# Kernel optimization log

Measured on AMD Instinct MI355X. Metric: run time of the kernel, lower is better.

The kernel has to match this reference:

```python
import jax, jax.numpy as jnp
import numpy as np

N, F, H, E = 20000, 512, 8, 320000
D = F // H
SCALING = D ** (-0.5)


def _layernorm(x, g, b, eps=1e-5):
    mu = jnp.mean(x, axis=-1, keepdims=True)
    var = jnp.var(x, axis=-1, keepdims=True)
    return (x - mu) * jax.lax.rsqrt(var + eps) * g + b


def setup_inputs() -> dict:
    key = jax.random.key(0)
    ks = jax.random.split(key, 12)
    feat = jax.random.normal(ks[0], (N, F), dtype=jnp.float32)
    edge_src = jax.random.randint(ks[1], (E,), 0, N, dtype=jnp.int32)
    edge_dst = jax.random.randint(ks[2], (E,), 0, N, dtype=jnp.int32)
    # self-loops on the first N edges so every node has in-degree >= 1
    loops = jnp.arange(N, dtype=jnp.int32)
    edge_src = edge_src.at[:N].set(loops)
    edge_dst = edge_dst.at[:N].set(loops)
    s = 1.0 / np.sqrt(F)
    def w(k, shape, scale=s):
        return jax.random.normal(k, shape, dtype=jnp.float32) * scale
    return {
        "feat": feat, "edge_src": edge_src, "edge_dst": edge_dst,
        "Wq": w(ks[3], (F, F)), "Wk": w(ks[4], (F, F)), "Wv": w(ks[5], (F, F)),
        "Wnode": w(ks[6], (F, F)), "Wskip": w(ks[7], (F, F)),
        "Wgate": w(ks[8], (3 * F, 1), scale=1.0 / np.sqrt(3 * F)),
        "ln1_g": jnp.ones((F,), jnp.float32), "ln1_b": jnp.zeros((F,), jnp.float32),
        "ln2_g": jnp.ones((F,), jnp.float32), "ln2_b": jnp.zeros((F,), jnp.float32),
        "W1": w(ks[9], (F, F)), "W2": w(ks[10], (F, F)),
    }


def reference(feat, edge_src, edge_dst, Wq, Wk, Wv, Wnode, Wskip, Wgate,
              ln1_g, ln1_b, ln2_g, ln2_b, W1, W2):
    # --- attention (GraphMultiAttentionV2, use_efeats=False, eval mode) ---
    q = (feat @ Wq).reshape(N, H, D)
    k = (feat @ Wk).reshape(N, H, D)
    v = (feat @ Wv).reshape(N, H, D)
    # u_dot_v: per-edge per-head dot product  [E, H]
    logits = jnp.einsum('ehd,ehd->eh', q[edge_src], k[edge_dst])
    logits = jnp.clip(logits, -5.0, 5.0) / SCALING  # faithful: a / scaling
    # edge softmax grouped by destination node
    m = jax.ops.segment_max(logits, edge_dst, num_segments=N)  # [N, H]
    ex = jnp.exp(logits - m[edge_dst])
    denom = jax.ops.segment_sum(ex, edge_dst, num_segments=N)
    sa = ex / denom[edge_dst]  # [E, H]
    # u_mul_e + sum aggregation
    msg = v[edge_src] * sa[..., None]  # [E, H, D]
    agg = jax.ops.segment_sum(msg, edge_dst, num_segments=N).reshape(N, F)
    rst = agg @ Wnode
    # --- gated residual ---
    skip = feat @ Wskip
    gate = jax.nn.sigmoid(jnp.concatenate([rst, skip, rst - skip], axis=-1) @ Wgate)
    h = _layernorm(rst * gate + skip * (1.0 - gate), ln1_g, ln1_b)
    # --- FFN + residual ---
    ffn = jax.nn.relu(_layernorm(h, ln2_g, ln2_b) @ W1) @ W2
    return h + ffn
```

## Files before the change

### kernel.cpp

```cpp
#include <hip/hip_runtime.h>
#include <hip/hip_bf16.h>
#include <hip/hip_fp16.h>

#define NN 20000
#define FD 512
#define NH 8
#define NE 320000
#define MP 20096

typedef unsigned int u32;
typedef unsigned short u16;
typedef __bf16 bf16x8 __attribute__((ext_vector_type(8)));
typedef _Float16 f16x8 __attribute__((ext_vector_type(8)));
typedef float f32x4 __attribute__((ext_vector_type(4)));

#define AS1 __attribute__((address_space(1)))
#define AS3 __attribute__((address_space(3)))

__device__ __forceinline__ u16 f2bf(float f) {
  __hip_bfloat16 h = __float2bfloat16(f);
  union { __hip_bfloat16 b; u16 u; } c; c.b = h; return c.u;
}
__device__ __forceinline__ float bf2f(u32 u) { return __uint_as_float(u << 16); }
__device__ __forceinline__ u16 f2h(float f) {
  union { __half h; u16 u; } c; c.h = __float2half(f); return c.u;
}
__device__ __forceinline__ void gl_lds16(const void* g, void* l) {
  __builtin_amdgcn_global_load_lds((AS1 void*)const_cast<void*>(g), (AS3 void*)l, 16, 0, 0);
}
__device__ __forceinline__ void up_h4(uint2 w, float* f) {
  union { u32 u; __half2 h; } c;
  c.u = w.x; float2 t0 = __half22float2(c.h); f[0]=t0.x; f[1]=t0.y;
  c.u = w.y; float2 t1 = __half22float2(c.h); f[2]=t1.x; f[3]=t1.y;
}

__global__ __launch_bounds__(256) void k_wprep(const float* __restrict__ feat,
    const float* __restrict__ Wq, const float* __restrict__ Wk,
    const float* __restrict__ Wv, const float* __restrict__ Wsk,
    const float* __restrict__ Wn, const float* __restrict__ W1,
    const float* __restrict__ W2, const float* __restrict__ Wg,
    const int* __restrict__ e_dst,
    u16* __restrict__ Af, u16* __restrict__ Bqkvs, u16* __restrict__ Bnt,
    u16* __restrict__ B1t, u16* __restrict__ B2t,
    float* __restrict__ gA, float* __restrict__ gB, int* __restrict__ deg)
{
  int idx = blockIdx.x * 256 + threadIdx.x;
  if (idx < MP * FD / 4) {
    size_t i = (size_t)idx * 4;
    float4 v = make_float4(0.f, 0.f, 0.f, 0.f);
    if (i < (size_t)NN * FD) v = *(const float4*)(feat + i);
    *(ushort4*)(Af + i) = make_ushort4(f2h(v.x), f2h(v.y), f2h(v.z), f2h(v.w));
    return;
  }
  idx -= MP * FD / 4;
  if (idx < 2048 * 512) {
    int n = idx >> 9, k = idx & 511;
    float v;
    if (n < 1024) {
      int j = n & 7, dim = (n >> 3) * 4 + (j & 3);
      v = (j < 4) ? Wq[k * 512 + dim] : Wv[k * 512 + dim];
    } else if (n < 1536) v = Wk[k * 512 + (n - 1024)];
    else                 v = Wsk[k * 512 + (n - 1536)];
    Bqkvs[idx] = f2h(v);
    return;
  }
  idx -= 2048 * 512;
  if (idx < 512 * 512) { int n = idx >> 9, k = idx & 511; Bnt[idx] = f2bf(Wn[k * 512 + n]); return; }
  idx -= 512 * 512;
  if (idx < 512 * 512) { int n = idx >> 9, k = idx & 511; B1t[idx] = f2bf(W1[k * 512 + n]); return; }
  idx -= 512 * 512;
  if (idx < 512 * 512) { int n = idx >> 9, k = idx & 511; B2t[idx] = f2bf(W2[k * 512 + n]); return; }
  idx -= 512 * 512;
  if (idx < 512) {
    gA[idx] = Wg[idx] + Wg[2 * 512 + idx];
    gB[idx] = Wg[512 + idx] - Wg[2 * 512 + idx];
    return;
  }
  idx -= 512;
  if (idx < NE) atomicAdd(&deg[e_dst[idx]], 1);
}

template<int NCOLS, int MODE, int FP16>
__global__ __launch_bounds__(256, 4) void k_gemm(
    const u16* __restrict__ A, const u16* __restrict__ B,
    float* __restrict__ Cf, u16* __restrict__ Cb, u16* __restrict__ Cb2,
    u16* __restrict__ Cb3, int Mreal)
{
  const long brow = (long)blockIdx.x * 128;
  if (brow >= MP) return;
  __shared__ u16 sA[2][128 * 32];
  __shared__ u16 sB[2][128 * 32];
  const int tid = threadIdx.x, lane = tid & 63, w = tid >> 6;
  const int wr = w >> 1, wc = w & 1;
  const long bcol = (long)blockIdx.y * 128;
  const int srl = tid >> 2, scl = (tid & 3) * 8;

  auto stage = [&](int b, int kt) {
#pragma unroll
    for (int s = 0; s < 2; s++) {
      gl_lds16(A + (brow + s * 64 + srl) * FD + kt + scl, &sA[b][s * 2048 + w * 512]);
      gl_lds16(B + (bcol + s * 64 + srl) * FD + kt + scl, &sB[b][s * 2048 + w * 512]);
    }
  };

  f32x4 acc[4][4] = {};
  stage(0, 0);
  __syncthreads();
  int cur = 0;
  const int ro = (lane >> 4) * 8;
  for (int kt = 0; kt < FD; kt += 32) {
    if (kt + 32 < FD) stage(cur ^ 1, kt + 32);
#pragma unroll
    for (int m = 0; m < 4; m++) {
      const u16* pa = &sA[cur][(wr * 64 + m * 16 + (lane & 15)) * 32 + ro];
#pragma unroll
      for (int n = 0; n < 4; n++) {
        const u16* pb = &sB[cur][(wc * 64 + n * 16 + (lane & 15)) * 32 + ro];
        if constexpr (FP16)
          acc[m][n] = __builtin_amdgcn_mfma_f32_16x16x32_f16(
              *(const f16x8*)pa, *(const f16x8*)pb, acc[m][n], 0, 0, 0);
        else
          acc[m][n] = __builtin_amdgcn_mfma_f32_16x16x32_bf16(
              *(const bf16x8*)pa, *(const bf16x8*)pb, acc[m][n], 0, 0, 0);
      }
    }
    __syncthreads();
    cur ^= 1;
  }
#pragma unroll
  for (int m = 0; m < 4; m++) {
    long row0 = brow + wr * 64 + m * 16 + (lane >> 4) * 4;
#pragma unroll
    for (int n = 0; n < 4; n++) {
      long col = bcol + wc * 64 + n * 16 + (lane & 15);
#pragma unroll
      for (int j = 0; j < 4; j++) {
        long row = row0 + j;
        if (row < Mreal) {
          float v = acc[m][n][j];
          if constexpr (MODE == 1) Cb[row * NCOLS + col] = f2bf(fmaxf(v, 0.f));
          else if constexpr (MODE == 2) Cb[row * NCOLS + col] = f2bf(v);
          else if constexpr (MODE == 6) {
            if (col < 1024)      Cb[row * 1024 + col] = f2h(v);
            else if (col < 1536) Cb2[row * 512 + (col - 1024)] = f2h(v);
            else                 Cb3[row * 512 + (col - 1536)] = f2bf(v);
          } else {
            long o = row * NCOLS + col;
            Cf[o] = bf2f((u32)Cb2[o]) + v;
          }
        }
      }
    }
  }
}

__global__ __launch_bounds__(1024) void k_scan(const int* __restrict__ deg, int* __restrict__ offa)
{
  __shared__ int wsum[16];
  const int tid = threadIdx.x, lane = tid & 63, wid = tid >> 6;
  const int base = tid * 20;
  int loc[20];
  int s = 0;
#pragma unroll
  for (int j = 0; j < 20; j++) {
    int i = base + j;
    int v = (i < NN) ? deg[i] : 0;
    s += v; loc[j] = s;
  }
  int incl = s;
#pragma unroll
  for (int d = 1; d < 64; d <<= 1) { int t = __shfl_up(incl, d); if (lane >= d) incl += t; }
  if (lane == 63) wsum[wid] = incl;
  __syncthreads();
  if (tid < 16) {
    int ws = wsum[tid];
#pragma unroll
    for (int d = 1; d < 16; d <<= 1) { int t = __shfl_up(ws, d, 16); if (tid >= d) ws += t; }
    wsum[tid] = ws;
  }
  __syncthreads();
  int prev = incl - s + (wid ? wsum[wid - 1] : 0);
  if (tid == 0) offa[0] = 0;
#pragma unroll
  for (int j = 0; j < 20; j++) {
    int i = base + j;
    if (i < NN) offa[i + 1] = prev + loc[j];
  }
}

__global__ __launch_bounds__(256) void k_scatter(const int* __restrict__ src, const int* __restrict__ dst,
    const int* __restrict__ offa, int* __restrict__ cnt, int* __restrict__ esrcs)
{
  int e = blockIdx.x * 256 + threadIdx.x;
  if (e >= NE) return;
  int d = dst[e];
  int p = offa[d] + atomicAdd(&cnt[d], 1);
  esrcs[p] = src[e];
}

__global__ __launch_bounds__(256) void k_edge(const int* __restrict__ offa,
    const int* __restrict__ esrcs, const u16* __restrict__ QV,
    const u16* __restrict__ Kb, u16* __restrict__ aggb)
{
  int wid = blockIdx.x * 4 + (threadIdx.x >> 6);
  int nd = wid >> 1, half = wid & 1;
  int lane = threadIdx.x & 63;
  if (nd >= MP) return;
  const int g = half * 64 + lane;
  u16* op = aggb + (size_t)nd * FD + g * 4;
  if (nd >= NN) { *(ushort4*)op = make_ushort4(0, 0, 0, 0); return; }
  uint2 kw = *(const uint2*)(Kb + (size_t)nd * 512 + g * 4);
  float kx[4]; up_h4(kw, kx);
  int b0 = offa[nd], b1 = offa[nd + 1];
  float den = 0.f, a0 = 0.f, a1 = 0.f, a2 = 0.f, a3 = 0.f;
  for (int p = b0; p < b1; p += 8) {
    int ss[8]; uint4 qv[8];
#pragma unroll
    for (int u = 0; u < 8; u++) { int ix = p + u; ss[u] = esrcs[ix < b1 ? ix : b1 - 1]; }
#pragma unroll
    for (int u = 0; u < 8; u++)
      qv[u] = *(const uint4*)(QV + (size_t)ss[u] * 1024 + g * 8);
#pragma unroll
    for (int u = 0; u < 8; u++) {
      float qx[4]; up_h4(make_uint2(qv[u].x, qv[u].y), qx);
      float d = qx[0]*kx[0] + qx[1]*kx[1] + qx[2]*kx[2] + qx[3]*kx[3];
      d += __shfl_xor(d, 1); d += __shfl_xor(d, 2);
      d += __shfl_xor(d, 4); d += __shfl_xor(d, 8);
      float ex = __expf(fminf(fmaxf(d, -5.f), 5.f) * 8.f - 40.f);
      ex = (p + u < b1) ? ex : 0.f;
      den += ex;
      float vx[4]; up_h4(make_uint2(qv[u].z, qv[u].w), vx);
      a0 += ex * vx[0]; a1 += ex * vx[1]; a2 += ex * vx[2]; a3 += ex * vx[3];
    }
  }
  float rd = 1.f / den;
  *(ushort4*)op = make_ushort4(f2bf(a0*rd), f2bf(a1*rd), f2bf(a2*rd), f2bf(a3*rd));
}

__device__ __forceinline__ float blkred(float v, float* sb)
{
#pragma unroll
  for (int s = 1; s < 64; s <<= 1) v += __shfl_xor(v, s);
  __syncthreads();
  if ((threadIdx.x & 63) == 0) sb[threadIdx.x >> 6] = v;
  __syncthreads();
  return sb[0] + sb[1];
}

__global__ __launch_bounds__(128) void k_gate_ln(const u16* __restrict__ rstb, const u16* __restrict__ skpb,
    const float* __restrict__ gA, const float* __restrict__ gB,
    const float* __restrict__ g1, const float* __restrict__ b1,
    const float* __restrict__ g2, const float* __restrict__ b2,
    u16* __restrict__ hb, u16* __restrict__ h2b)
{
  __shared__ float sb[2];
  const int t = threadIdx.x;
  const size_t base = (size_t)blockIdx.x * FD + t * 4;
  ushort4 ru = *(const ushort4*)(rstb + base);
  ushort4 su = *(const ushort4*)(skpb + base);
  float r0 = bf2f(ru.x), r1 = bf2f(ru.y), r2 = bf2f(ru.z), r3 = bf2f(ru.w);
  float s0 = bf2f(su.x), s1 = bf2f(su.y), s2 = bf2f(su.z), s3 = bf2f(su.w);
  float4 av = *(const float4*)(gA + t * 4);
  float4 bv = *(const float4*)(gB + t * 4);
  float gd = r0*av.x + r1*av.y + r2*av.z + r3*av.w
           + s0*bv.x + s1*bv.y + s2*bv.z + s3*bv.w;
  float tot = blkred(gd, sb);
  float g = 1.f / (1.f + __expf(-tot));
  float x0 = g*r0 + (1.f-g)*s0;
  float x1 = g*r1 + (1.f-g)*s1;
  float x2 = g*r2 + (1.f-g)*s2;
  float x3 = g*r3 + (1.f-g)*s3;
  float m1 = blkred(x0+x1+x2+x3, sb) * (1.f/FD);
  float d0 = x0-m1, d1 = x1-m1, d2 = x2-m1, d3 = x3-m1;
  float v1 = blkred(d0*d0+d1*d1+d2*d2+d3*d3, sb) * (1.f/FD);
  float rs = rsqrtf(v1 + 1e-5f);
  float4 G1 = *(const float4*)(g1 + t*4);
  float4 Bb1 = *(const float4*)(b1 + t*4);
  float h0 = d0*rs*G1.x + Bb1.x;
  float h1 = d1*rs*G1.y + Bb1.y;
  float h2 = d2*rs*G1.z + Bb1.z;
  float h3 = d3*rs*G1.w + Bb1.w;
  *(ushort4*)(hb + base) = make_ushort4(f2bf(h0), f2bf(h1), f2bf(h2), f2bf(h3));
  float m2 = blkred(h0+h1+h2+h3, sb) * (1.f/FD);
  float e0 = h0-m2, e1 = h1-m2, e2 = h2-m2, e3 = h3-m2;
  float v2 = blkred(e0*e0+e1*e1+e2*e2+e3*e3, sb) * (1.f/FD);
  float rs2 = rsqrtf(v2 + 1e-5f);
  float4 G2 = *(const float4*)(g2 + t*4);
  float4 Bb2 = *(const float4*)(b2 + t*4);
  *(ushort4*)(h2b + base) = make_ushort4(
      f2bf(e0*rs2*G2.x + Bb2.x), f2bf(e1*rs2*G2.y + Bb2.y),
      f2bf(e2*rs2*G2.z + Bb2.z), f2bf(e3*rs2*G2.w + Bb2.w));
}

extern "C" void kernel_launch(void* const* d_in, const int* in_sizes, int n_in,
                              void* d_out, int out_size, void* d_ws, size_t ws_size,
                              hipStream_t stream)
{
  const float* feat = (const float*)d_in[0];
  const int* e_src = (const int*)d_in[1];
  const int* e_dst = (const int*)d_in[2];
  const float* Wq  = (const float*)d_in[3];
  const float* Wk  = (const float*)d_in[4];
  const float* Wv  = (const float*)d_in[5];
  const float* Wn  = (const float*)d_in[6];
  const float* Wsk = (const float*)d_in[7];
  const float* Wg  = (const float*)d_in[8];
  const float* l1g = (const float*)d_in[9];
  const float* l1b = (const float*)d_in[10];
  const float* l2g = (const float*)d_in[11];
  const float* l2b = (const float*)d_in[12];
  const float* W1  = (const float*)d_in[13];
  const float* W2  = (const float*)d_in[14];

  char* ws = (char*)d_ws;
  size_t o = 0;
  auto al = [&](size_t b) { char* r = ws + o; o = (o + b + 255) & ~(size_t)255; return r; };

  u16* Af    = (u16*)al((size_t)MP * FD * 2);
  u16* Bqkvs = (u16*)al((size_t)2048 * FD * 2);
  u16* Bnt   = (u16*)al((size_t)FD * FD * 2);
  u16* B1t   = (u16*)al((size_t)FD * FD * 2);
  u16* B2t   = (u16*)al((size_t)FD * FD * 2);
  float* gA  = (float*)al(FD * 4);
  float* gB  = (float*)al(FD * 4);
  u16* QV    = (u16*)al((size_t)MP * 1024 * 2);
  u16* Kb    = (u16*)al((size_t)MP * FD * 2);
  u16* SKIPb = (u16*)al((size_t)MP * FD * 2);
  u16* aggb  = (u16*)al((size_t)MP * FD * 2);
  u16* h2b   = (u16*)al((size_t)MP * FD * 2);
  u16* hb    = (u16*)al((size_t)MP * FD * 2);
  int* deg   = (int*)al((size_t)2 * NN * 4);
  int* cnt   = deg + NN;
  int* offa  = (int*)al((size_t)(NN + 1) * 4);
  int* esrcs = (int*)al((size_t)NE * 4);
  if (o > ws_size) return;
  u16* rstb = Kb;
  u16* midb = Af;
  float* out = (float*)d_out;

  hipMemsetAsync(deg, 0, (size_t)2 * NN * 4, stream);

  {
    int total = MP * FD / 4 + 2048 * 512 + 3 * 512 * 512 + 512 + NE;
    k_wprep<<<dim3((total + 255) / 256), 256, 0, stream>>>(feat, Wq, Wk, Wv, Wsk, Wn, W1, W2, Wg,
        e_dst, Af, Bqkvs, Bnt, B1t, B2t, gA, gB, deg);
  }

  k_gemm<2048, 6, 1><<<dim3(160, 16), 256, 0, stream>>>(Af, Bqkvs, nullptr, QV, Kb, SKIPb, MP);

  k_scan<<<dim3(1), 1024, 0, stream>>>(deg, offa);
  k_scatter<<<dim3((NE + 255) / 256), 256, 0, stream>>>(e_src, e_dst, offa, cnt, esrcs);
  k_edge<<<dim3(MP / 2), 256, 0, stream>>>(offa, esrcs, QV, Kb, aggb);

  k_gemm<512, 2, 0><<<dim3(160, 4), 256, 0, stream>>>(aggb, Bnt, nullptr, rstb, nullptr, nullptr, MP);
  k_gate_ln<<<dim3(NN), 128, 0, stream>>>(rstb, SKIPb, gA, gB, l1g, l1b, l2g, l2b, hb, h2b);
  k_gemm<512, 1, 0><<<dim3(160, 4), 256, 0, stream>>>(h2b, B1t, nullptr, midb, nullptr, nullptr, NN);
  k_gemm<512, 7, 0><<<dim3(160, 4), 256, 0, stream>>>(midb, B2t, out, nullptr, hb, nullptr, NN);
}
```

Measured before the change: 315.7 us.

## Fold second layernorm into W1 GEMM epilogue and use wave-per-row gate LN

The second layernorm is folded algebraically into the FFN's first GEMM. W1 is pre-scaled by ln2 gamma, per-row rstd and rstd*mean are computed in the gate kernel, and the GEMM epilogue applies rs*acc - rs*mean*(g·W1) + (b·W1). This removes the h2b write and read. The gate/LN kernel is also restructured so one wavefront handles a row with shuffle-only reductions and single-pass mean/variance, replacing 128-thread blocks with repeated block barriers. The trade-offs are more bf16 rounding error, since h is rounded before the GEMM while the statistics come from fp32, and a serial 512-length dot-product loop added to the prep kernel.

```diff
diff --git a/kernel.cpp b/kernel.cpp
--- a/kernel.cpp
+++ b/kernel.cpp
@@ -33,16 +33,24 @@
   c.u = w.x; float2 t0 = __half22float2(c.h); f[0]=t0.x; f[1]=t0.y;
   c.u = w.y; float2 t1 = __half22float2(c.h); f[2]=t1.x; f[3]=t1.y;
 }
+__device__ __forceinline__ void up_b8(uint4 w, float* f) {
+  f[0]=bf2f(w.x & 0xffffu); f[1]=bf2f(w.x >> 16);
+  f[2]=bf2f(w.y & 0xffffu); f[3]=bf2f(w.y >> 16);
+  f[4]=bf2f(w.z & 0xffffu); f[5]=bf2f(w.z >> 16);
+  f[6]=bf2f(w.w & 0xffffu); f[7]=bf2f(w.w >> 16);
+}
 
 __global__ __launch_bounds__(256) void k_wprep(const float* __restrict__ feat,
     const float* __restrict__ Wq, const float* __restrict__ Wk,
     const float* __restrict__ Wv, const float* __restrict__ Wsk,
     const float* __restrict__ Wn, const float* __restrict__ W1,
     const float* __restrict__ W2, const float* __restrict__ Wg,
+    const float* __restrict__ l2g, const float* __restrict__ l2b,
     const int* __restrict__ e_dst,
     u16* __restrict__ Af, u16* __restrict__ Bqkvs, u16* __restrict__ Bnt,
     u16* __restrict__ B1t, u16* __restrict__ B2t,
-    float* __restrict__ gA, float* __restrict__ gB, int* __restrict__ deg)
+    float* __restrict__ gA, float* __restrict__ gB,
+    float* __restrict__ uw, int* __restrict__ deg)
 {
   int idx = blockIdx.x * 256 + threadIdx.x;
   if (idx < MP * FD / 4) {
@@ -67,7 +75,8 @@
   idx -= 2048 * 512;
   if (idx < 512 * 512) { int n = idx >> 9, k = idx & 511; Bnt[idx] = f2bf(Wn[k * 512 + n]); return; }
   idx -= 512 * 512;
-  if (idx < 512 * 512) { int n = idx >> 9, k = idx & 511; B1t[idx] = f2bf(W1[k * 512 + n]); return; }
+  if (idx < 512 * 512) { int n = idx >> 9, k = idx & 511;
+    B1t[idx] = f2bf(l2g[k] * W1[k * 512 + n]); return; }
   idx -= 512 * 512;
   if (idx < 512 * 512) { int n = idx >> 9, k = idx & 511; B2t[idx] = f2bf(W2[k * 512 + n]); return; }
   idx -= 512 * 512;
@@ -77,6 +86,15 @@
     return;
   }
   idx -= 512;
+  if (idx < 1024) {
+    int j = idx & 511;
+    const float* vec = (idx < 512) ? l2g : l2b;
+    float acc = 0.f;
+    for (int c = 0; c < 512; c++) acc += vec[c] * W1[c * 512 + j];
+    uw[idx] = acc;
+    return;
+  }
+  idx -= 1024;
   if (idx < NE) atomicAdd(&deg[e_dst[idx]], 1);
 }
 
@@ -127,6 +145,7 @@
     __syncthreads();
     cur ^= 1;
   }
+  const float* uwp = (const float*)Cb2;
 #pragma unroll
   for (int m = 0; m < 4; m++) {
     long row0 = brow + wr * 64 + m * 16 + (lane >> 4) * 4;
@@ -138,15 +157,17 @@
         long row = row0 + j;
         if (row < Mreal) {
           float v = acc[m][n][j];
-          if constexpr (MODE == 1) Cb[row * NCOLS + col] = f2bf(fmaxf(v, 0.f));
-          else if constexpr (MODE == 2) Cb[row * NCOLS + col] = f2bf(v);
+          if constexpr (MODE == 2) Cb[row * NCOLS + col] = f2bf(v);
           else if constexpr (MODE == 6) {
             if (col < 1024)      Cb[row * 1024 + col] = f2h(v);
             else if (col < 1536) Cb2[row * 512 + (col - 1024)] = f2h(v);
             else                 Cb3[row * 512 + (col - 1536)] = f2bf(v);
-          } else {
+          } else if constexpr (MODE == 7) {
             long o = row * NCOLS + col;
             Cf[o] = bf2f((u32)Cb2[o]) + v;
+          } else {
+            float val = Cf[row] * v - Cf[NN + row] * uwp[col] + uwp[512 + col];
+            Cb[row * NCOLS + col] = f2bf(fmaxf(val, 0.f));
           }
         }
       }
@@ -237,59 +258,67 @@
   *(ushort4*)op = make_ushort4(f2bf(a0*rd), f2bf(a1*rd), f2bf(a2*rd), f2bf(a3*rd));
 }
 
-__device__ __forceinline__ float blkred(float v, float* sb)
-{
-#pragma unroll
-  for (int s = 1; s < 64; s <<= 1) v += __shfl_xor(v, s);
-  __syncthreads();
-  if ((threadIdx.x & 63) == 0) sb[threadIdx.x >> 6] = v;
-  __syncthreads();
-  return sb[0] + sb[1];
-}
-
-__global__ __launch_bounds__(128) void k_gate_ln(const u16* __restrict__ rstb, const u16* __restrict__ skpb,
-    const float* __restrict__ gA, const float* __restrict__ gB,
+__global__ __launch_bounds__(256) void k_gate_ln(const u16* __restrict__ rstb,
+    const u16* __restrict__ skpb, const float* __restrict__ gA, const float* __restrict__ gB,
     const float* __restrict__ g1, const float* __restrict__ b1,
-    const float* __restrict__ g2, const float* __restrict__ b2,
-    u16* __restrict__ hb, u16* __restrict__ h2b)
-{
-  __shared__ float sb[2];
-  const int t = threadIdx.x;
-  const size_t base = (size_t)blockIdx.x * FD + t * 4;
-  ushort4 ru = *(const ushort4*)(rstb + base);
-  ushort4 su = *(const ushort4*)(skpb + base);
-  float r0 = bf2f(ru.x), r1 = bf2f(ru.y), r2 = bf2f(ru.z), r3 = bf2f(ru.w);
-  float s0 = bf2f(su.x), s1 = bf2f(su.y), s2 = bf2f(su.z), s3 = bf2f(su.w);
-  float4 av = *(const float4*)(gA + t * 4);
-  float4 bv = *(const float4*)(gB + t * 4);
-  float gd = r0*av.x + r1*av.y + r2*av.z + r3*av.w
-           + s0*bv.x + s1*bv.y + s2*bv.z + s3*bv.w;
-  float tot = blkred(gd, sb);
-  float g = 1.f / (1.f + __expf(-tot));
-  float x0 = g*r0 + (1.f-g)*s0;
-  float x1 = g*r1 + (1.f-g)*s1;
-  float x2 = g*r2 + (1.f-g)*s2;
-  float x3 = g*r3 + (1.f-g)*s3;
-  float m1 = blkred(x0+x1+x2+x3, sb) * (1.f/FD);
-  float d0 = x0-m1, d1 = x1-m1, d2 = x2-m1, d3 = x3-m1;
-  float v1 = blkred(d0*d0+d1*d1+d2*d2+d3*d3, sb) * (1.f/FD);
+    u16* __restrict__ hb, float* __restrict__ scal)
+{
+  int nd = blockIdx.x * 4 + (threadIdx.x >> 6);
+  int lane = threadIdx.x & 63;
+  if (nd >= NN) return;
+  const size_t base = (size_t)nd * FD + lane * 8;
+  float r[8], s[8], a[8], b[8];
+  up_b8(*(const uint4*)(rstb + base), r);
+  up_b8(*(const uint4*)(skpb + base), s);
+  *(float4*)&a[0] = *(const float4*)(gA + lane * 8);
+  *(float4*)&a[4] = *(const float4*)(gA + lane * 8 + 4);
+  *(float4*)&b[0] = *(const float4*)(gB + lane * 8);
+  *(float4*)&b[4] = *(const float4*)(gB + lane * 8 + 4);
+  float gd = 0.f;
+#pragma unroll
+  for (int i = 0; i < 8; i++) gd += r[i] * a[i] + s[i] * b[i];
+#pragma unroll
+  for (int d = 1; d < 64; d <<= 1) gd += __shfl_xor(gd, d);
+  float g = 1.f / (1.f + __expf(-gd));
+  float x[8], sx = 0.f, sxx = 0.f;
+#pragma unroll
+  for (int i = 0; i < 8; i++) {
+    x[i] = g * r[i] + (1.f - g) * s[i];
+    sx += x[i]; sxx += x[i] * x[i];
+  }
+#pragma unroll
+  for (int d = 1; d < 64; d <<= 1) { sx += __shfl_xor(sx, d); sxx += __shfl_xor(sxx, d); }
+  float m1 = sx * (1.f / FD);
+  float v1 = sxx * (1.f / FD) - m1 * m1;
   float rs = rsqrtf(v1 + 1e-5f);
-  float4 G1 = *(const float4*)(g1 + t*4);
-  float4 Bb1 = *(const float4*)(b1 + t*4);
-  float h0 = d0*rs*G1.x + Bb1.x;
-  float h1 = d1*rs*G1.y + Bb1.y;
-  float h2 = d2*rs*G1.z + Bb1.z;
-  float h3 = d3*rs*G1.w + Bb1.w;
-  *(ushort4*)(hb + base) = make_ushort4(f2bf(h0), f2bf(h1), f2bf(h2), f2bf(h3));
-  float m2 = blkred(h0+h1+h2+h3, sb) * (1.f/FD);
-  float e0 = h0-m2, e1 = h1-m2, e2 = h2-m2, e3 = h3-m2;
-  float v2 = blkred(e0*e0+e1*e1+e2*e2+e3*e3, sb) * (1.f/FD);
-  float rs2 = rsqrtf(v2 + 1e-5f);
-  float4 G2 = *(const float4*)(g2 + t*4);
-  float4 Bb2 = *(const float4*)(b2 + t*4);
-  *(ushort4*)(h2b + base) = make_ushort4(
-      f2bf(e0*rs2*G2.x + Bb2.x), f2bf(e1*rs2*G2.y + Bb2.y),
-      f2bf(e2*rs2*G2.z + Bb2.z), f2bf(e3*rs2*G2.w + Bb2.w));
+  float G1[8], Bb1[8];
+  *(float4*)&G1[0] = *(const float4*)(g1 + lane * 8);
+  *(float4*)&G1[4] = *(const float4*)(g1 + lane * 8 + 4);
+  *(float4*)&Bb1[0] = *(const float4*)(b1 + lane * 8);
+  *(float4*)&Bb1[4] = *(const float4*)(b1 + lane * 8 + 4);
+  float h[8], sh = 0.f, shh = 0.f;
+  u16 ho[8];
+#pragma unroll
+  for (int i = 0; i < 8; i++) {
+    h[i] = (x[i] - m1) * rs * G1[i] + Bb1[i];
+    sh += h[i]; shh += h[i] * h[i];
+    ho[i] = f2bf(h[i]);
+  }
+  uint4 st;
+  st.x = (u32)ho[0] | ((u32)ho[1] << 16);
+  st.y = (u32)ho[2] | ((u32)ho[3] << 16);
+  st.z = (u32)ho[4] | ((u32)ho[5] << 16);
+  st.w = (u32)ho[6] | ((u32)ho[7] << 16);
+  *(uint4*)(hb + base) = st;
+#pragma unroll
+  for (int d = 1; d < 64; d <<= 1) { sh += __shfl_xor(sh, d); shh += __shfl_xor(shh, d); }
+  if (lane == 0) {
+    float m2 = sh * (1.f / FD);
+    float v2 = shh * (1.f / FD) - m2 * m2;
+    float rs2 = rsqrtf(v2 + 1e-5f);
+    scal[nd] = rs2;
+    scal[NN + nd] = rs2 * m2;
+  }
 }
 
 extern "C" void kernel_launch(void* const* d_in, const int* in_sizes, int n_in,
@@ -323,12 +352,13 @@
   u16* B2t   = (u16*)al((size_t)FD * FD * 2);
   float* gA  = (float*)al(FD * 4);
   float* gB  = (float*)al(FD * 4);
+  float* uw  = (float*)al(1024 * 4);
   u16* QV    = (u16*)al((size_t)MP * 1024 * 2);
   u16* Kb    = (u16*)al((size_t)MP * FD * 2);
   u16* SKIPb = (u16*)al((size_t)MP * FD * 2);
   u16* aggb  = (u16*)al((size_t)MP * FD * 2);
-  u16* h2b   = (u16*)al((size_t)MP * FD * 2);
   u16* hb    = (u16*)al((size_t)MP * FD * 2);
+  float* scal= (float*)al((size_t)2 * NN * 4);
   int* deg   = (int*)al((size_t)2 * NN * 4);
   int* cnt   = deg + NN;
   int* offa  = (int*)al((size_t)(NN + 1) * 4);
@@ -341,9 +371,9 @@
   hipMemsetAsync(deg, 0, (size_t)2 * NN * 4, stream);
 
   {
-    int total = MP * FD / 4 + 2048 * 512 + 3 * 512 * 512 + 512 + NE;
+    int total = MP * FD / 4 + 2048 * 512 + 3 * 512 * 512 + 512 + 1024 + NE;
     k_wprep<<<dim3((total + 255) / 256), 256, 0, stream>>>(feat, Wq, Wk, Wv, Wsk, Wn, W1, W2, Wg,
-        e_dst, Af, Bqkvs, Bnt, B1t, B2t, gA, gB, deg);
+        l2g, l2b, e_dst, Af, Bqkvs, Bnt, B1t, B2t, gA, gB, uw, deg);
   }
 
   k_gemm<2048, 6, 1><<<dim3(160, 16), 256, 0, stream>>>(Af, Bqkvs, nullptr, QV, Kb, SKIPb, MP);
@@ -353,7 +383,7 @@
   k_edge<<<dim3(MP / 2), 256, 0, stream>>>(offa, esrcs, QV, Kb, aggb);
 
   k_gemm<512, 2, 0><<<dim3(160, 4), 256, 0, stream>>>(aggb, Bnt, nullptr, rstb, nullptr, nullptr, MP);
-  k_gate_ln<<<dim3(NN), 128, 0, stream>>>(rstb, SKIPb, gA, gB, l1g, l1b, l2g, l2b, hb, h2b);
-  k_gemm<512, 1, 0><<<dim3(160, 4), 256, 0, stream>>>(h2b, B1t, nullptr, midb, nullptr, nullptr, NN);
+  k_gate_ln<<<dim3((NN + 3) / 4), 256, 0, stream>>>(rstb, SKIPb, gA, gB, l1g, l1b, hb, scal);
+  k_gemm<512, 8, 0><<<dim3(160, 4), 256, 0, stream>>>(hb, B1t, scal, midb, (u16*)uw, nullptr, NN);
   k_gemm<512, 7, 0><<<dim3(160, 4), 256, 0, stream>>>(midb, B2t, out, nullptr, hb, nullptr, NN);
 }
```

Result: slower. 330.1 us (+4.6%).
